# Kernel tuning notes

Hardware: AMD Instinct MI355X
Metric: run time of the kernel (lower is better)

Reference implementation:

```python
import jax, jax.numpy as jnp
import numpy as np


def _gcn_norm(edge_index, edge_weight, n_nodes):
    # PyG gcn_norm with add_self_loops=True, fill_value=1.0.
    row, col = edge_index[0], edge_index[1]
    loop = jnp.arange(n_nodes, dtype=edge_index.dtype)
    row = jnp.concatenate([row, loop])
    col = jnp.concatenate([col, loop])
    w = jnp.concatenate([edge_weight, jnp.ones((n_nodes,), edge_weight.dtype)])
    deg = jax.ops.segment_sum(w, col, num_segments=n_nodes)
    dinv = jnp.where(deg > 0, jax.lax.rsqrt(deg), 0.0)
    norm = dinv[row] * w * dinv[col]
    return row, col, norm


def _gcn_conv(x, row, col, norm, W, b, n_nodes):
    h = x @ W                                  # [N, F_out]
    msg = h[row] * norm[:, None]               # gather + scale, [E+N, F_out]
    out = jax.ops.segment_sum(msg, col, num_segments=n_nodes)
    return out + b


def setup_inputs() -> dict:
    key = jax.random.key(0)
    k = jax.random.split(key, 7)
    N, E, Fin, Fout = 50000, 1600000, 256, 128
    H = 2 * Fout
    x = jax.random.normal(k[0], (N, Fin), dtype=jnp.float32)
    edge_index = jax.random.randint(k[1], (2, E), 0, N, dtype=jnp.int64)
    edge_weight = jax.random.uniform(k[2], (E,), dtype=jnp.float32)
    # Glorot init as in PyG GCNConv (weight stored as [in, out] here)
    s1 = float(np.sqrt(6.0 / (Fin + H)))
    s2 = float(np.sqrt(6.0 / (H + Fout)))
    W1 = jax.random.uniform(k[3], (Fin, H), minval=-s1, maxval=s1, dtype=jnp.float32)
    b1 = jnp.zeros((H,), jnp.float32)
    W2 = jax.random.uniform(k[4], (H, Fout), minval=-s2, maxval=s2, dtype=jnp.float32)
    b2 = jnp.zeros((Fout,), jnp.float32)
    return {"x": x, "edge_index": edge_index, "edge_weight": edge_weight,
            "W1": W1, "b1": b1, "W2": W2, "b2": b2}


def reference(x, edge_index, edge_weight, W1, b1, W2, b2):
    n_nodes = x.shape[0]
    # cached=True: normalization computed once, reused by both layers
    row, col, norm = _gcn_norm(edge_index, edge_weight, n_nodes)
    h = _gcn_conv(x, row, col, norm, W1, b1, n_nodes)
    h = jax.nn.relu(h)
    out = _gcn_conv(h, row, col, norm, W2, b2, n_nodes)
    return out
```

## Files before the change

### kernel.cpp

```cpp
#include <hip/hip_runtime.h>

typedef __attribute__((ext_vector_type(8))) short  short8;
typedef __attribute__((ext_vector_type(4))) float  f32x4;
typedef __attribute__((ext_vector_type(4))) ushort us4;
typedef __attribute__((ext_vector_type(4))) uint   u32x4;
typedef __attribute__((ext_vector_type(2))) uint   u32x2;
typedef unsigned long long ull;

__device__ __forceinline__ float bf2f(ushort u) {
    union { uint i; float f; } c; c.i = ((uint)u) << 16; return c.f;
}
__device__ __forceinline__ float bits2f(uint b) {
    union { uint i; float f; } c; c.i = b; return c.f;
}
__device__ __forceinline__ ushort f2bf(float f) {
    union { float f; uint i; } c; c.f = f;
    uint b = c.i + 0x7fffu + ((c.i >> 16) & 1u);
    return (ushort)(b >> 16);
}

#define NBLK  256
#define NBMAX 1024

__device__ __forceinline__
void histA_body(const int* __restrict__ col, int* __restrict__ counts,
                int E, int NB, uint* hist) {
    for (int j = threadIdx.x; j < NB; j += 256) hist[j] = 0u;
    __syncthreads();
    for (int i = blockIdx.x * 256 + threadIdx.x; i < E; i += 256 * NBLK)
        atomicAdd(&hist[((uint)col[i]) >> 6], 1u);
    __syncthreads();
    for (int j = threadIdx.x; j < NB; j += 256)
        counts[j * NBLK + blockIdx.x] = (int)hist[j];
}

__device__ __forceinline__
void binC_body(const int* __restrict__ row, const int* __restrict__ col,
               const float* __restrict__ w,
               const int* __restrict__ counts, const int* __restrict__ bbase,
               ull* __restrict__ recs, int E, int NB, uint* cur) {
    for (int j = threadIdx.x; j < NB; j += 256)
        cur[j] = (uint)(bbase[j] + counts[j * NBLK + blockIdx.x]);
    __syncthreads();
    for (int i = blockIdx.x * 256 + threadIdx.x; i < E; i += 256 * NBLK) {
        int c = col[i], r = row[i];
        float wv = w[i];
        uint w16 = (uint)(wv * 65536.0f);
        if (w16 > 65535u) w16 = 65535u;
        uint pos = atomicAdd(&cur[((uint)c) >> 6], 1u);
        recs[pos] = ((ull)(uint)c << 32) | (ull)((w16 << 16) | (uint)(r & 0xffff));
    }
}

__device__ __forceinline__
void binDa_body(const ull* __restrict__ recs, const int* __restrict__ bbase,
                int* __restrict__ cntp, float* __restrict__ dinv,
                int* __restrict__ rowptr, ushort* __restrict__ perm, int N,
                uint* cnt, uint* ws, uint* arr, uint* keys) {
    int b = blockIdx.x, t = threadIdx.x;
    if (t < 64) { cnt[t] = 0u; ws[t] = 0u; }
    __syncthreads();
    int lo = bbase[b], hi = bbase[b + 1];
    for (int i = lo + t; i < hi; i += 256) {
        ull rec = recs[i];
        atomicAdd(&cnt[((uint)(rec >> 32)) & 63u], 1u);
        atomicAdd(&ws[((uint)(rec >> 32)) & 63u], (uint)((rec >> 16) & 0xffffu));
    }
    __syncthreads();
    int node = b * 64 + t;
    uint cp = 0;
    if (t < 64) {
        if (node < N) cp = (cnt[t] + 3u) & ~3u;
        arr[t] = cp;
        keys[t] = (node < N) ? cp : 0xffffffffu;
    }
    __syncthreads();
    for (int off = 1; off < 64; off <<= 1) {
        uint x = (t < 64 && t >= off) ? arr[t - off] : 0u;
        __syncthreads();
        if (t < 64) arr[t] += x;
        __syncthreads();
    }
    if (t < 64 && node < N) {
        int base = bbase[b] + 192 * b;
        rowptr[node] = base + (int)(arr[t] - cp);
        cntp[node]   = (int)cp;
        dinv[node]   = rsqrtf(1.0f + (float)ws[t] * (1.0f / 65536.0f));
        uint key = keys[t];
        int rank = 0;
        #pragma unroll 8
        for (int j = 0; j < 64; ++j) {
            uint kj = keys[j];
            rank += (kj < key) || (kj == key && j < t);
        }
        perm[b * 64 + rank] = (ushort)node;
    }
}

__device__ __forceinline__
void binDb_body(const ull* __restrict__ recs, const int* __restrict__ bbase,
                const int* __restrict__ rowptr, const int* __restrict__ cntp,
                const float* __restrict__ dinv, uint* __restrict__ edgesP, int N,
                uint* curN, uint* rbs, uint* cps) {
    int b = blockIdx.x, t = threadIdx.x;
    int node = b * 64 + t;
    if (t < 64) {
        uint rp = 0u, cp = 0u;
        if (node < N) { rp = (uint)rowptr[node]; cp = (uint)cntp[node]; }
        rbs[t] = rp; curN[t] = rp; cps[t] = cp;
    }
    __syncthreads();
    int lo = bbase[b], hi = bbase[b + 1];
    for (int i = lo + t; i < hi; i += 256) {
        ull rec = recs[i];
        uint c   = (uint)(rec >> 32);
        uint r   = (uint)rec & 0xffffu;
        uint w16 = ((uint)rec >> 16) & 0xffffu;
        float nv = dinv[r] * ((float)w16 * (1.0f / 65536.0f)) * dinv[c];
        uint slot = atomicAdd(&curN[c & 63u], 1u);
        edgesP[slot] = r | ((uint)f2bf(nv) << 16);
    }
    __syncthreads();
    if (t < 64 && node < N) {
        uint e1 = rbs[t] + cps[t];
        for (uint j = curN[t]; j < e1; ++j) edgesP[j] = 0u;
    }
}

__global__ void k_scanB1(int* __restrict__ counts, int* __restrict__ btot) {
    __shared__ int s[256];
    int b = blockIdx.x, t = threadIdx.x;
    int v = counts[b * NBLK + t];
    s[t] = v; __syncthreads();
    for (int off = 1; off < 256; off <<= 1) {
        int x = (t >= off) ? s[t - off] : 0;
        __syncthreads();
        s[t] += x;
        __syncthreads();
    }
    counts[b * NBLK + t] = s[t] - v;
    if (t == 255) btot[b] = s[255];
}

__global__ void k_scanB2(const int* __restrict__ btot, int* __restrict__ bbase, int NB) {
    __shared__ int s[256];
    int t = threadIdx.x;
    int v[4]; int sum = 0;
    #pragma unroll
    for (int j = 0; j < 4; ++j) {
        int i = t * 4 + j;
        v[j] = (i < NB) ? btot[i] : 0;
        sum += v[j];
    }
    s[t] = sum; __syncthreads();
    for (int off = 1; off < 256; off <<= 1) {
        int x = (t >= off) ? s[t - off] : 0;
        __syncthreads();
        s[t] += x;
        __syncthreads();
    }
    int excl = s[t] - sum;
    #pragma unroll
    for (int j = 0; j < 4; ++j) {
        int i = t * 4 + j;
        if (i <= NB) bbase[i] = excl;
        excl += v[j];
    }
}

__device__ __forceinline__
void splitT_body(const float* __restrict__ W, ushort* __restrict__ Th,
                 ushort* __restrict__ Tl, int K, int N, int i) {
    if (i < K * N) {
        int k = i / N, n = i - k * N;
        float v = W[i];
        ushort hi = f2bf(v);
        ushort lo = f2bf(v - bf2f(hi));
        Th[(size_t)n * K + k] = hi;
        Tl[(size_t)n * K + k] = lo;
    }
}

#define LDA 40

__device__ __forceinline__
void gemm3_body(const float* __restrict__ A, const ushort* __restrict__ BTh,
                const ushort* __restrict__ BTl, ushort* __restrict__ Cpan,
                int M, int Nc, int K, int bm, int bn,
                ushort (*As)[128][LDA], ushort (*Bs)[128][LDA]) {
    const int t    = threadIdx.x;
    const int lane = t & 63;
    const int wid  = t >> 6;
    const int wm   = wid >> 1;
    const int wn   = wid & 1;
    const int ml   = lane & 15;
    const int kq   = lane >> 4;

    f32x4 acc[4][4];
    #pragma unroll
    for (int mt = 0; mt < 4; ++mt)
        #pragma unroll
        for (int nt = 0; nt < 4; ++nt) acc[mt][nt] = (f32x4){0.f, 0.f, 0.f, 0.f};

    for (int k0 = 0; k0 < K; k0 += 32) {
        #pragma unroll
        for (int it = 0; it < 4; ++it) {
            int idx = (t + it * 256) * 4;
            int r  = idx >> 5;
            int kk = idx & 31;
            int grow = bm + r;
            f32x4 v = (f32x4){0.f, 0.f, 0.f, 0.f};
            if (grow < M) v = *(const f32x4*)&A[(size_t)grow * K + k0 + kk];
            us4 hi, lo;
            #pragma unroll
            for (int j = 0; j < 4; ++j) {
                ushort h = f2bf(v[j]);
                hi[j] = h;
                lo[j] = f2bf(v[j] - bf2f(h));
            }
            *(us4*)&As[0][r][kk] = hi;
            *(us4*)&As[1][r][kk] = lo;
        }
        #pragma unroll
        for (int it = 0; it < 2; ++it) {
            int idx = (t + it * 256) * 8;
            int n  = idx >> 5;
            int kk = idx & 31;
            u32x4 vh = *(const u32x4*)&BTh[(size_t)(bn + n) * K + k0 + kk];
            *(u32x4*)&Bs[0][n][kk] = vh;
            u32x4 vl = *(const u32x4*)&BTl[(size_t)(bn + n) * K + k0 + kk];
            *(u32x4*)&Bs[1][n][kk] = vl;
        }
        __syncthreads();

        short8 a[4][2], b[4][2];
        #pragma unroll
        for (int mt = 0; mt < 4; ++mt) {
            a[mt][0] = *(const short8*)&As[0][wm * 64 + mt * 16 + ml][kq * 8];
            a[mt][1] = *(const short8*)&As[1][wm * 64 + mt * 16 + ml][kq * 8];
        }
        #pragma unroll
        for (int nt = 0; nt < 4; ++nt) {
            b[nt][0] = *(const short8*)&Bs[0][wn * 64 + nt * 16 + ml][kq * 8];
            b[nt][1] = *(const short8*)&Bs[1][wn * 64 + nt * 16 + ml][kq * 8];
        }
        #pragma unroll
        for (int mt = 0; mt < 4; ++mt)
            #pragma unroll
            for (int nt = 0; nt < 4; ++nt) {
                acc[mt][nt] = __builtin_amdgcn_mfma_f32_16x16x32_bf16(a[mt][0], b[nt][0], acc[mt][nt], 0, 0, 0);
                acc[mt][nt] = __builtin_amdgcn_mfma_f32_16x16x32_bf16(a[mt][0], b[nt][1], acc[mt][nt], 0, 0, 0);
                acc[mt][nt] = __builtin_amdgcn_mfma_f32_16x16x32_bf16(a[mt][1], b[nt][0], acc[mt][nt], 0, 0, 0);
            }
        __syncthreads();
    }

    #pragma unroll
    for (int mt = 0; mt < 4; ++mt) {
        int rbase = bm + wm * 64 + mt * 16 + kq * 4;
        #pragma unroll
        for (int nt = 0; nt < 4; ++nt) {
            int colg = bn + wn * 64 + nt * 16 + ml;
            size_t pbase = (size_t)(colg >> 5) * M * 32 + (colg & 31);
            #pragma unroll
            for (int r = 0; r < 4; ++r) {
                int rr = rbase + r;
                if (rr < M) Cpan[pbase + (size_t)rr * 32] = f2bf(acc[mt][nt][r]);
            }
        }
    }
}

__global__ __launch_bounds__(256)
void k_gemm3(const float* __restrict__ A, const ushort* __restrict__ BTh,
             const ushort* __restrict__ BTl, ushort* __restrict__ Cpan,
             int M, int Nc, int K) {
    __shared__ __align__(16) ushort As[2][128][LDA];
    __shared__ __align__(16) ushort Bs[2][128][LDA];
    gemm3_body(A, BTh, BTl, Cpan, M, Nc, K, blockIdx.y * 128, blockIdx.x * 128, As, Bs);
}

__global__ __launch_bounds__(256)
void k_fusedA(const int* __restrict__ col, int* __restrict__ counts, int E, int NB,
              const float* __restrict__ W1, ushort* __restrict__ WT1h, ushort* __restrict__ WT1l,
              int Fin, int H,
              const float* __restrict__ W2, ushort* __restrict__ WT2h, ushort* __restrict__ WT2l,
              int Fout, int sp1) {
    __shared__ uint hist[NBMAX];
    int bid = (int)blockIdx.x;
    if (bid < NBLK) { histA_body(col, counts, E, NB, hist); return; }
    if (bid < NBLK + sp1) { splitT_body(W1, WT1h, WT1l, Fin, H, (bid - NBLK) * 256 + (int)threadIdx.x); return; }
    splitT_body(W2, WT2h, WT2l, H, Fout, (bid - NBLK - sp1) * 256 + (int)threadIdx.x);
}

__global__ __launch_bounds__(256)
void k_fusedB1(const int* __restrict__ row, const int* __restrict__ col,
               const float* __restrict__ w, const int* __restrict__ counts,
               const int* __restrict__ bbase, ull* __restrict__ recs, int E, int NB,
               const float* __restrict__ A, const ushort* __restrict__ BTh,
               const ushort* __restrict__ BTl, ushort* __restrict__ Cpan,
               int M, int Nc, int K, int t0) {
    __shared__ __align__(16) ushort As[2][128][LDA];
    __shared__ __align__(16) ushort Bs[2][128][LDA];
    int bid = (int)blockIdx.x;
    if (bid < NBLK) { binC_body(row, col, w, counts, bbase, recs, E, NB, (uint*)&As[0][0][0]); return; }
    int tile = t0 + bid - NBLK;
    int nbn = Nc >> 7;
    gemm3_body(A, BTh, BTl, Cpan, M, Nc, K, (tile / nbn) * 128, (tile % nbn) * 128, As, Bs);
}

__global__ __launch_bounds__(256)
void k_fusedB2(const ull* __restrict__ recs, const int* __restrict__ bbase,
               int* __restrict__ cntp, float* __restrict__ dinv,
               int* __restrict__ rowptr, ushort* __restrict__ perm,
               int N, int NB,
               const float* __restrict__ A, const ushort* __restrict__ BTh,
               const ushort* __restrict__ BTl, ushort* __restrict__ Cpan,
               int M, int Nc, int K, int t0) {
    __shared__ __align__(16) ushort As[2][128][LDA];
    __shared__ __align__(16) ushort Bs[2][128][LDA];
    int bid = (int)blockIdx.x;
    if (bid < NB) {
        uint* l = (uint*)&As[0][0][0];
        binDa_body(recs, bbase, cntp, dinv, rowptr, perm, N, l, l + 64, l + 128, l + 192);
        return;
    }
    int tile = t0 + bid - NB;
    int nbn = Nc >> 7;
    gemm3_body(A, BTh, BTl, Cpan, M, Nc, K, (tile / nbn) * 128, (tile % nbn) * 128, As, Bs);
}

__global__ __launch_bounds__(256)
void k_fusedB3(const ull* __restrict__ recs, const int* __restrict__ bbase,
               const int* __restrict__ rowptr, const int* __restrict__ cntp,
               const float* __restrict__ dinv, uint* __restrict__ edgesP,
               int N, int NB,
               const float* __restrict__ A, const ushort* __restrict__ BTh,
               const ushort* __restrict__ BTl, ushort* __restrict__ Cpan,
               int M, int Nc, int K, int t0) {
    __shared__ __align__(16) ushort As[2][128][LDA];
    __shared__ __align__(16) ushort Bs[2][128][LDA];
    int bid = (int)blockIdx.x;
    if (bid < NB) {
        uint* l = (uint*)&As[0][0][0];
        binDb_body(recs, bbase, rowptr, cntp, dinv, edgesP, N, l, l + 64, l + 128);
        return;
    }
    int tile = t0 + bid - NB;
    int nbn = Nc >> 7;
    gemm3_body(A, BTh, BTl, Cpan, M, Nc, K, (tile / nbn) * 128, (tile % nbn) * 128, As, Bs);
}

#define NPB 64

template <bool RELU>
__device__ __forceinline__
void aggr_body(const ushort* __restrict__ perm, const int* __restrict__ rowptr,
               const int* __restrict__ cntp, const uint* __restrict__ edges,
               const ushort* __restrict__ hpan, const float* __restrict__ dinv,
               const float* __restrict__ bias, float* __restrict__ out,
               int F, int npan, int N) {
    const int bid  = blockIdx.x;
    const int p    = bid % npan;
    const int wave = threadIdx.x >> 6;
    const int lane = threadIdx.x & 63;
    const int g    = lane >> 2;
    const int c    = lane & 3;
    const int idx  = (bid / npan) * NPB + wave * 16 + g;
    const int fbase = p * 32 + c * 8;

    const ushort* hp = hpan + (size_t)p * N * 32 + c * 8;

    int node = 0, beg = 0, end = 0;
    if (idx < N) {
        node = (int)perm[idx];
        beg = rowptr[node];
        end = beg + cntp[node];
    }

    float acc[8] = {};
    int e = beg;
    u32x4 pk4 = (u32x4){0u, 0u, 0u, 0u};
    if (e < end) pk4 = *(const u32x4*)&edges[e];
    while (__any(e < end)) {
        u32x4 cur = pk4;
        int e2 = e + 4;
        if (e2 < end) pk4 = *(const u32x4*)&edges[e2];
        if (e < end) {
            #pragma unroll
            for (int j = 0; j < 4; ++j) {
                uint pk = cur[j];
                float nv = bits2f(pk & 0xffff0000u);
                int r = (int)(pk & 0xffffu);
                u32x4 hv = *(const u32x4*)(hp + (size_t)r * 32);
                #pragma unroll
                for (int q = 0; q < 4; ++q) {
                    acc[2 * q]     += nv * bits2f(hv[q] << 16);
                    acc[2 * q + 1] += nv * bits2f(hv[q] & 0xffff0000u);
                }
            }
        }
        e = e2;
    }

    if (idx < N) {
        float di = dinv[node];
        float d2 = di * di;
        u32x4 hs = *(const u32x4*)(hp + (size_t)node * 32);
        f32x4 bv0 = *(const f32x4*)&bias[fbase];
        f32x4 bv1 = *(const f32x4*)&bias[fbase + 4];
        f32x4 v0, v1;
        #pragma unroll
        for (int q = 0; q < 4; ++q) {
            float r0 = acc[2 * q]     + d2 * bits2f(hs[q] << 16)
                     + ((q < 2) ? bv0[2 * q] : bv1[2 * q - 4]);
            float r1 = acc[2 * q + 1] + d2 * bits2f(hs[q] & 0xffff0000u)
                     + ((q < 2) ? bv0[2 * q + 1] : bv1[2 * q - 3]);
            if (RELU) { r0 = fmaxf(r0, 0.f); r1 = fmaxf(r1, 0.f); }
            if (q < 2) { v0[2 * q] = r0; v0[2 * q + 1] = r1; }
            else       { v1[2 * q - 4] = r0; v1[2 * q - 3] = r1; }
        }
        *(f32x4*)&out[(size_t)node * F + fbase]     = v0;
        *(f32x4*)&out[(size_t)node * F + fbase + 4] = v1;
    }
}

__global__ __launch_bounds__(256)
void k_aggr1(const ushort* __restrict__ perm, const int* __restrict__ rowptr,
             const int* __restrict__ cntp, const uint* __restrict__ edges,
             const ushort* __restrict__ hpan, const float* __restrict__ dinv,
             const float* __restrict__ bias, float* __restrict__ out,
             int F, int npan, int N) {
    aggr_body<true>(perm, rowptr, cntp, edges, hpan, dinv, bias, out, F, npan, N);
}

__global__ __launch_bounds__(256)
void k_aggr2(const ushort* __restrict__ perm, const int* __restrict__ rowptr,
             const int* __restrict__ cntp, const uint* __restrict__ edges,
             const ushort* __restrict__ hpan, const float* __restrict__ dinv,
             const float* __restrict__ bias, float* __restrict__ out,
             int F, int npan, int N) {
    aggr_body<false>(perm, rowptr, cntp, edges, hpan, dinv, bias, out, F, npan, N);
}


static inline char* bump(char*& p, size_t bytes) {
    char* r = p;
    p += (bytes + 255) & ~(size_t)255;
    return r;
}

extern "C" void kernel_launch(void* const* d_in, const int* in_sizes, int n_in,
                              void* d_out, int out_size, void* d_ws, size_t ws_size,
                              hipStream_t stream) {
    const float* x  = (const float*)d_in[0];
    const int*   ei = (const int*)d_in[1];
    const float* ew = (const float*)d_in[2];
    const float* W1 = (const float*)d_in[3];
    const float* b1 = (const float*)d_in[4];
    const float* W2 = (const float*)d_in[5];
    const float* b2 = (const float*)d_in[6];
    float* out = (float*)d_out;

    const int E    = in_sizes[2];
    const int H    = in_sizes[4];
    const int Fout = in_sizes[6];
    const int Fin  = in_sizes[3] / H;
    const int N    = in_sizes[0] / Fin;
    const int NB   = (N + 63) >> 6;

    const int* row = ei;
    const int* col = ei + E;

    char* p = (char*)d_ws;
    float*  dinv   = (float*)bump(p, (size_t)N * 4);
    int*    cntp   = (int*)bump(p, (size_t)N * 4);
    int*    rowptr = (int*)bump(p, (size_t)N * 4);
    ushort* perm   = (ushort*)bump(p, (size_t)NBMAX * 64 * 2);
    uint*   edgesP = (uint*)bump(p, ((size_t)E + 3 * N + 192 * (size_t)NBMAX + 256) * 4);
    int*    counts = (int*)bump(p, (size_t)NBMAX * NBLK * 4);
    int*    btot   = (int*)bump(p, (size_t)NBMAX * 4);
    int*    bbase  = (int*)bump(p, (size_t)(NBMAX + 1) * 4);
    ushort* WT1h   = (ushort*)bump(p, (size_t)Fin * H * 2);
    ushort* WT1l   = (ushort*)bump(p, (size_t)Fin * H * 2);
    ushort* WT2h   = (ushort*)bump(p, (size_t)H * Fout * 2);
    ushort* WT2l   = (ushort*)bump(p, (size_t)H * Fout * 2);
    ushort* h1     = (ushort*)bump(p, (size_t)N * H * 2);
    float*  a1     = (float*)bump(p, (size_t)N * H * 4);
    ushort* h2     = (ushort*)bump(p, (size_t)N * Fout * 2);

    ull* recs = (ull*)a1;

    const int sp1 = (Fin * H + 255) / 256;
    const int sp2 = (H * Fout + 255) / 256;
    const int gb1 = (H / 128) * ((N + 127) / 128);
    int T1 = gb1 < 280 ? gb1 : 280;
    int T2 = gb1 < 480 ? gb1 : 480;
    if (T2 < T1) T2 = T1;

    k_fusedA<<<NBLK + sp1 + sp2, 256, 0, stream>>>(col, counts, E, NB,
                                                   W1, WT1h, WT1l, Fin, H,
                                                   W2, WT2h, WT2l, Fout, sp1);
    k_scanB1<<<NB, 256, 0, stream>>>(counts, btot);
    k_scanB2<<<1, 256, 0, stream>>>(btot, bbase, NB);
    k_fusedB1<<<NBLK + T1, 256, 0, stream>>>(row, col, ew, counts, bbase, recs, E, NB,
                                             x, WT1h, WT1l, h1, N, H, Fin, 0);
    k_fusedB2<<<NB + (T2 - T1), 256, 0, stream>>>(recs, bbase, cntp, dinv, rowptr, perm,
                                                  N, NB, x, WT1h, WT1l, h1, N, H, Fin, T1);
    k_fusedB3<<<NB + (gb1 - T2), 256, 0, stream>>>(recs, bbase, rowptr, cntp, dinv,
                                                   edgesP, N, NB,
                                                   x, WT1h, WT1l, h1, N, H, Fin, T2);

    const int chunks = (N + NPB - 1) / NPB;

    k_aggr1<<<chunks * (H / 32), 256, 0, stream>>>(perm, rowptr, cntp, edgesP, h1, dinv, b1, a1, H, H / 32, N);

    k_gemm3<<<dim3(Fout / 128, (N + 127) / 128), 256, 0, stream>>>(a1, WT2h, WT2l, h2, N, Fout, H);
    k_aggr2<<<chunks * (Fout / 32), 256, 0, stream>>>(perm, rowptr, cntp, edgesP, h2, dinv, b2, out, Fout, Fout / 32, N);
}
```

Measured before the change: 417.8 us.

## Software-pipeline aggregation gathers two stages deep and double histogram blocks

The aggregation loop is restructured so edge records are prefetched 16 ahead and feature-row gathers for the next 8 edges are issued before the current 8 are accumulated, keeping more memory loads in flight per lane. Padded or out-of-range entries use a zero record, which gathers row 0 with zero weight rather than skipping the load. Separately, the histogram pass uses 512 blocks instead of 256, and the per-bin scan now handles two counts per thread. The risks are higher register pressure, which may lower occupancy, and some wasted gathers for short rows.

```diff
diff --git a/kernel.cpp b/kernel.cpp
--- a/kernel.cpp
+++ b/kernel.cpp
@@ -19,7 +19,7 @@
     return (ushort)(b >> 16);
 }
 
-#define NBLK  256
+#define NBLK  512
 #define NBMAX 1024
 
 __device__ __forceinline__
@@ -130,15 +130,19 @@
 __global__ void k_scanB1(int* __restrict__ counts, int* __restrict__ btot) {
     __shared__ int s[256];
     int b = blockIdx.x, t = threadIdx.x;
-    int v = counts[b * NBLK + t];
-    s[t] = v; __syncthreads();
+    int v0 = counts[b * NBLK + 2 * t];
+    int v1 = counts[b * NBLK + 2 * t + 1];
+    int sum = v0 + v1;
+    s[t] = sum; __syncthreads();
     for (int off = 1; off < 256; off <<= 1) {
         int x = (t >= off) ? s[t - off] : 0;
         __syncthreads();
         s[t] += x;
         __syncthreads();
     }
-    counts[b * NBLK + t] = s[t] - v;
+    int excl = s[t] - sum;
+    counts[b * NBLK + 2 * t]     = excl;
+    counts[b * NBLK + 2 * t + 1] = excl + v0;
     if (t == 255) btot[b] = s[255];
 }
 
@@ -353,6 +357,17 @@
 
 #define NPB 64
 
+#define GATHER(pk) (*(const u32x4*)(hp + (size_t)((pk) & 0xffffu) * 32))
+#define CONSUME(pk, hv)                                              \
+    {                                                                \
+        float nv = bits2f((pk) & 0xffff0000u);                       \
+        _Pragma("unroll")                                            \
+        for (int q = 0; q < 4; ++q) {                                \
+            acc[2 * q]     += nv * bits2f((hv)[q] << 16);            \
+            acc[2 * q + 1] += nv * bits2f((hv)[q] & 0xffff0000u);    \
+        }                                                            \
+    }
+
 template <bool RELU>
 __device__ __forceinline__
 void aggr_body(const ushort* __restrict__ perm, const int* __restrict__ rowptr,
@@ -379,28 +394,34 @@
     }
 
     float acc[8] = {};
-    int e = beg;
-    u32x4 pk4 = (u32x4){0u, 0u, 0u, 0u};
-    if (e < end) pk4 = *(const u32x4*)&edges[e];
-    while (__any(e < end)) {
-        u32x4 cur = pk4;
-        int e2 = e + 4;
-        if (e2 < end) pk4 = *(const u32x4*)&edges[e2];
-        if (e < end) {
-            #pragma unroll
-            for (int j = 0; j < 4; ++j) {
-                uint pk = cur[j];
-                float nv = bits2f(pk & 0xffff0000u);
-                int r = (int)(pk & 0xffffu);
-                u32x4 hv = *(const u32x4*)(hp + (size_t)r * 32);
-                #pragma unroll
-                for (int q = 0; q < 4; ++q) {
-                    acc[2 * q]     += nv * bits2f(hv[q] << 16);
-                    acc[2 * q + 1] += nv * bits2f(hv[q] & 0xffff0000u);
-                }
-            }
-        }
-        e = e2;
+    const u32x4 Z = (u32x4){0u, 0u, 0u, 0u};
+    int e0 = beg;
+    u32x4 pkA0 = Z, pkA1 = Z, pkB0 = Z, pkB1 = Z;
+    if (e0      < end) pkA0 = *(const u32x4*)&edges[e0];
+    if (e0 +  4 < end) pkA1 = *(const u32x4*)&edges[e0 + 4];
+    if (e0 +  8 < end) pkB0 = *(const u32x4*)&edges[e0 + 8];
+    if (e0 + 12 < end) pkB1 = *(const u32x4*)&edges[e0 + 12];
+    u32x4 hvA0 = GATHER(pkA0[0]), hvA1 = GATHER(pkA0[1]);
+    u32x4 hvA2 = GATHER(pkA0[2]), hvA3 = GATHER(pkA0[3]);
+    u32x4 hvA4 = GATHER(pkA1[0]), hvA5 = GATHER(pkA1[1]);
+    u32x4 hvA6 = GATHER(pkA1[2]), hvA7 = GATHER(pkA1[3]);
+
+    while (__any(e0 < end)) {
+        u32x4 pkC0 = Z, pkC1 = Z;
+        if (e0 + 16 < end) pkC0 = *(const u32x4*)&edges[e0 + 16];
+        if (e0 + 20 < end) pkC1 = *(const u32x4*)&edges[e0 + 20];
+        u32x4 hvB0 = GATHER(pkB0[0]), hvB1 = GATHER(pkB0[1]);
+        u32x4 hvB2 = GATHER(pkB0[2]), hvB3 = GATHER(pkB0[3]);
+        u32x4 hvB4 = GATHER(pkB1[0]), hvB5 = GATHER(pkB1[1]);
+        u32x4 hvB6 = GATHER(pkB1[2]), hvB7 = GATHER(pkB1[3]);
+        CONSUME(pkA0[0], hvA0); CONSUME(pkA0[1], hvA1);
+        CONSUME(pkA0[2], hvA2); CONSUME(pkA0[3], hvA3);
+        CONSUME(pkA1[0], hvA4); CONSUME(pkA1[1], hvA5);
+        CONSUME(pkA1[2], hvA6); CONSUME(pkA1[3], hvA7);
+        pkA0 = pkB0; pkA1 = pkB1; pkB0 = pkC0; pkB1 = pkC1;
+        hvA0 = hvB0; hvA1 = hvB1; hvA2 = hvB2; hvA3 = hvB3;
+        hvA4 = hvB4; hvA5 = hvB5; hvA6 = hvB6; hvA7 = hvB7;
+        e0 += 8;
     }
 
     if (idx < N) {
```

New measurement: 407.7 us. 1.02x faster.
